# Kernel tuning notes

Hardware: AMD Instinct MI355X
Metric: run time of the kernel (lower is better)

The kernel has to match this reference:

```python
import jax, jax.numpy as jnp
import numpy as np

B, S, HID = 2, 2048, 1024
H, HKV, D = 16, 8, 128
G = H // HKV
EPS = 1e-6
ROPE_BASE = 1e6


def _rms_norm(x, w):
    # per-last-dim RMSNorm in fp32, matching QwenRMSNorm
    x32 = x.astype(jnp.float32)
    var = jnp.mean(x32 * x32, axis=-1, keepdims=True)
    return w * (x32 * jax.lax.rsqrt(var + EPS)).astype(x.dtype)


def _rotate_half(x):
    half = x.shape[-1] // 2
    return jnp.concatenate([-x[..., half:], x[..., :half]], axis=-1)


def setup_inputs() -> dict:
    key = jax.random.key(0)
    ks = jax.random.split(key, 6)
    return {
        "hidden_states": jax.random.normal(ks[0], (B, S, HID), dtype=jnp.float32),
        "position_ids": jnp.arange(S, dtype=jnp.int32),
        "Wq": jax.random.normal(ks[1], (HID, H * D), dtype=jnp.float32) * 0.02,
        "Wk": jax.random.normal(ks[2], (HID, HKV * D), dtype=jnp.float32) * 0.02,
        "Wv": jax.random.normal(ks[3], (HID, HKV * D), dtype=jnp.float32) * 0.02,
        "Wo": jax.random.normal(ks[4], (H * D, HID), dtype=jnp.float32) * 0.02,
        "q_norm_w": jnp.ones((D,), dtype=jnp.float32),
        "k_norm_w": jnp.ones((D,), dtype=jnp.float32),
    }


def reference(hidden_states, position_ids, Wq, Wk, Wv, Wo, q_norm_w, k_norm_w):
    b, s, _ = hidden_states.shape
    # projections
    q = (hidden_states @ Wq).reshape(b, s, H, D)
    k = (hidden_states @ Wk).reshape(b, s, HKV, D)
    v = (hidden_states @ Wv).reshape(b, s, HKV, D)
    # QK RMSNorm (per head_dim), then [B, heads, S, D]
    q = _rms_norm(q, q_norm_w).transpose(0, 2, 1, 3)
    k = _rms_norm(k, k_norm_w).transpose(0, 2, 1, 3)
    v = v.transpose(0, 2, 1, 3)
    # RoPE
    inv_freq = 1.0 / (ROPE_BASE ** (jnp.arange(0, D, 2, dtype=jnp.float32) / D))
    freqs = position_ids.astype(jnp.float32)[:, None] * inv_freq[None, :]  # [S, D/2]
    emb = jnp.concatenate([freqs, freqs], axis=-1)  # [S, D]
    cos = jnp.cos(emb)[None, None, :, :].astype(q.dtype)
    sin = jnp.sin(emb)[None, None, :, :].astype(q.dtype)
    q = q * cos + _rotate_half(q) * sin
    k = k * cos + _rotate_half(k) * sin
    # GQA attention without materializing repeated K/V:
    # q heads h = kh*G + g  <->  repeat_interleave(G, dim=1) of kv heads
    qg = q.reshape(b, HKV, G, s, D)
    scale = 1.0 / jnp.sqrt(jnp.asarray(D, dtype=q.dtype))
    scores = jnp.einsum('bhgqd,bhkd->bhgqk', qg, k) * scale  # [B,HKV,G,S,S]
    causal = jnp.tril(jnp.ones((s, s), dtype=bool))
    scores = jnp.where(causal[None, None, None, :, :], scores, jnp.finfo(scores.dtype).min)
    probs = jax.nn.softmax(scores, axis=-1)
    attn = jnp.einsum('bhgqk,bhkd->bhgqd', probs, v)  # [B,HKV,G,S,D]
    attn = attn.reshape(b, H, s, D).transpose(0, 2, 1, 3).reshape(b, s, H * D)
    out = attn @ Wo
    return out, k, v
```

## Files before the change

### kernel.cpp

```cpp
#include <hip/hip_runtime.h>

#define B_ 2
#define S_ 2048
#define HID_ 1024
#define H_ 16
#define HKV_ 8
#define D_ 128

typedef unsigned short u16;
typedef __attribute__((ext_vector_type(8))) short short8;
typedef __attribute__((ext_vector_type(4))) float f32x4;
typedef __attribute__((ext_vector_type(16))) float f32x16;
typedef __attribute__((ext_vector_type(2))) unsigned short u16x2;
typedef __attribute__((ext_vector_type(4))) unsigned short u16x4;
typedef const __attribute__((address_space(1))) void gvoid;
typedef __attribute__((address_space(3))) void svoid;

__device__ __forceinline__ u16 f2b(float f) {
  union { float f; unsigned u; } v; v.f = f;
  unsigned r = v.u + 0x7FFFu + ((v.u >> 16) & 1u);
  return (u16)(r >> 16);
}
__device__ __forceinline__ float b2f(u16 x) {
  union { unsigned u; float f; } v; v.u = ((unsigned)x) << 16; return v.f;
}

__device__ __forceinline__ float exp2_fast(float x) {
  float r; asm("v_exp_f32 %0, %1" : "=v"(r) : "v"(x)); return r;
}
__device__ __forceinline__ unsigned cvtpk_bf16(float lo, float hi) {
  unsigned r; asm("v_cvt_pk_bf16_f32 %0, %1, %2" : "=v"(r) : "v"(lo), "v"(hi)); return r;
}
__device__ __forceinline__ void vm_drain() {
  asm volatile("s_waitcnt vmcnt(0)" ::: "memory");
  __builtin_amdgcn_sched_barrier(0);
}

__global__ __launch_bounds__(256) void conv_bf16_kernel(const float* __restrict__ X,
                                                        u16* __restrict__ Y, int n4) {
  int i = blockIdx.x * 256 + threadIdx.x;
  if (i < n4) {
    const float4 v = ((const float4*)X)[i];
    u16x4 o = { f2b(v.x), f2b(v.y), f2b(v.z), f2b(v.w) };
    ((u16x4*)Y)[i] = o;
  }
}

template <bool PERM>
__global__ __launch_bounds__(256) void transpose_bf16_kernel(const float* __restrict__ W,
                                                             u16* __restrict__ Wt,
                                                             int K, int N) {
  __shared__ float t[32][33];
  const int nb = N >> 5;
  const int bx = blockIdx.x % nb;
  const int by = blockIdx.x / nb;
  const int tx = threadIdx.x & 31, ty = threadIdx.x >> 5;
#pragma unroll
  for (int i = 0; i < 32; i += 8)
    t[ty + i][tx] = W[(size_t)(by * 32 + ty + i) * N + bx * 32 + tx];
  __syncthreads();
#pragma unroll
  for (int i = 0; i < 32; i += 8) {
    int n = bx * 32 + ty + i;
    int nn;
    if (PERM) {
      int head = n >> 7, d = n & 127;
      int p = (d & 15) | (((d >> 6) & 1) << 4) | (((d >> 4) & 1) << 5) | (((d >> 5) & 1) << 6);
      nn = head * 128 + p;
    } else {
      nn = n;
    }
    Wt[(size_t)nn * K + by * 32 + tx] = f2b(t[tx][ty + i]);
  }
}

__global__ __launch_bounds__(256) void rope_table_kernel(const int* __restrict__ pid,
                                                         float* __restrict__ ct,
                                                         float* __restrict__ st) {
  int i = blockIdx.x * 256 + threadIdx.x;
  if (i >= 64 * S_) return;
  int f = i >> 11, s = i & 2047;
  double inv = exp2(-(double)f * (19.931568569324174 / 64.0));
  double ang = (double)pid[s] * inv;
  ct[i] = (float)cos(ang);
  st[i] = (float)sin(ang);
}

template <int M, int N, int K, int BM>
__global__ __launch_bounds__(256) void gemm_bt(const u16* __restrict__ A,
                                               const u16* __restrict__ Bt,
                                               float* __restrict__ C) {
  __shared__ u16 As[BM * 32];
  __shared__ u16 Bs[128 * 32];
  const int tid = threadIdx.x;
  const int w = tid >> 6;
  const int l = tid & 63;
  const int l15 = l & 15, lg = l >> 4;
  const int nbx = N / 128;
  const int bx = blockIdx.x % nbx, by = blockIdx.x / nbx;
  const int row0 = by * BM, col0 = bx * 128;
  const int wr = w >> 1, wc = w & 1;
  constexpr int MR = BM / 32;

  f32x4 acc[MR][4];
#pragma unroll
  for (int m = 0; m < MR; ++m)
#pragma unroll
    for (int n = 0; n < 4; ++n) acc[m][n] = (f32x4){0.f, 0.f, 0.f, 0.f};

  for (int k0 = 0; k0 < K; k0 += 32) {
    __syncthreads();
#pragma unroll
    for (int i = 0; i < BM / 64; ++i) {
      int c = i * 256 + tid;
      int r = c >> 2, cc = c & 3;
      const u16* sa = A + (size_t)(row0 + r) * K + k0 + cc * 8;
      __builtin_amdgcn_global_load_lds((gvoid*)sa, (svoid*)(As + (i * 256 + w * 64) * 8), 16, 0, 0);
    }
#pragma unroll
    for (int i = 0; i < 2; ++i) {
      int c = i * 256 + tid;
      int r = c >> 2, cc = c & 3;
      const u16* sb = Bt + (size_t)(col0 + r) * K + k0 + cc * 8;
      __builtin_amdgcn_global_load_lds((gvoid*)sb, (svoid*)(Bs + (i * 256 + w * 64) * 8), 16, 0, 0);
    }
    vm_drain();
    __syncthreads();
    short8 af[MR], bf[4];
#pragma unroll
    for (int m = 0; m < MR; ++m)
      af[m] = *(const short8*)(As + (wr * (BM / 2) + m * 16 + l15) * 32 + lg * 8);
#pragma unroll
    for (int n = 0; n < 4; ++n)
      bf[n] = *(const short8*)(Bs + (wc * 64 + n * 16 + l15) * 32 + lg * 8);
#pragma unroll
    for (int m = 0; m < MR; ++m)
#pragma unroll
      for (int n = 0; n < 4; ++n)
        acc[m][n] = __builtin_amdgcn_mfma_f32_16x16x32_bf16(af[m], bf[n], acc[m][n], 0, 0, 0);
  }
#pragma unroll
  for (int m = 0; m < MR; ++m)
#pragma unroll
    for (int n = 0; n < 4; ++n) {
      float* cp = C + (size_t)(row0 + wr * (BM / 2) + m * 16 + lg * 4) * N + col0 + wc * 64 + n * 16 + l15;
#pragma unroll
      for (int r = 0; r < 4; ++r) cp[(size_t)r * N] = acc[m][n][r];
    }
}

__global__ __launch_bounds__(256) void gemm_qkv_fused(const u16* __restrict__ A,
                                                      const u16* __restrict__ Bt,
                                                      const float* __restrict__ qnw,
                                                      const float* __restrict__ knw,
                                                      const float* __restrict__ ct_t,
                                                      const float* __restrict__ st_t,
                                                      u16* __restrict__ Qbb,
                                                      u16* __restrict__ Kbb,
                                                      float* __restrict__ kout,
                                                      float* __restrict__ vout,
                                                      u16* __restrict__ VTb) {
  constexpr int K = 1024;
  __shared__ u16 As[64 * 64];
  __shared__ u16 Bs[128 * 64];
  __shared__ float red[64][2];
  const int tid = threadIdx.x;
  const int w = tid >> 6;
  const int l = tid & 63;
  const int l15 = l & 15, lg = l >> 4;
  const int bx = blockIdx.x & 31, by = blockIdx.x >> 5;
  const int row0 = by * 64, col0 = bx * 128;
  const int wr = w >> 1, wc = w & 1;

  f32x4 acc[2][4];
#pragma unroll
  for (int m = 0; m < 2; ++m)
#pragma unroll
    for (int n = 0; n < 4; ++n) acc[m][n] = (f32x4){0.f, 0.f, 0.f, 0.f};

  for (int k0 = 0; k0 < K; k0 += 64) {
    __syncthreads();
#pragma unroll
    for (int i = 0; i < 2; ++i) {
      int c = i * 256 + tid;
      int r = c >> 3, cc = c & 7;
      int cs = cc ^ ((r ^ (r >> 3)) & 7);
      const u16* sa = A + (size_t)(row0 + r) * K + k0 + cs * 8;
      __builtin_amdgcn_global_load_lds((gvoid*)sa, (svoid*)(As + (i * 256 + w * 64) * 8), 16, 0, 0);
    }
#pragma unroll
    for (int i = 0; i < 4; ++i) {
      int c = i * 256 + tid;
      int r = c >> 3, cc = c & 7;
      int cs = cc ^ ((r ^ (r >> 3)) & 7);
      const u16* sb = Bt + (size_t)(col0 + r) * K + k0 + cs * 8;
      __builtin_amdgcn_global_load_lds((gvoid*)sb, (svoid*)(Bs + (i * 256 + w * 64) * 8), 16, 0, 0);
    }
    vm_drain();
    __syncthreads();
#pragma unroll
    for (int kk = 0; kk < 2; ++kk) {
      short8 af[2], bf[4];
#pragma unroll
      for (int m = 0; m < 2; ++m) {
        const int row = wr * 32 + m * 16 + l15;
        af[m] = *(const short8*)((const char*)As + row * 128 +
                                 (((kk * 4 + lg) ^ ((row ^ (row >> 3)) & 7)) << 4));
      }
#pragma unroll
      for (int n = 0; n < 4; ++n) {
        const int row = wc * 64 + n * 16 + l15;
        bf[n] = *(const short8*)((const char*)Bs + row * 128 +
                                 (((kk * 4 + lg) ^ ((row ^ (row >> 3)) & 7)) << 4));
      }
#pragma unroll
      for (int m = 0; m < 2; ++m)
#pragma unroll
        for (int n = 0; n < 4; ++n)
          acc[m][n] = __builtin_amdgcn_mfma_f32_16x16x32_bf16(af[m], bf[n], acc[m][n], 0, 0, 0);
    }
  }

  const int b_ = row0 >> 11;
  const int s0 = row0 & 2047;
  if (bx < 24) {
    float part[2][4];
#pragma unroll
    for (int m = 0; m < 2; ++m)
#pragma unroll
      for (int r = 0; r < 4; ++r) {
        float p = 0.f;
#pragma unroll
        for (int n = 0; n < 4; ++n) p += acc[m][n][r] * acc[m][n][r];
        part[m][r] = p;
      }
#pragma unroll
    for (int i = 1; i < 16; i <<= 1)
#pragma unroll
      for (int m = 0; m < 2; ++m)
#pragma unroll
        for (int r = 0; r < 4; ++r) part[m][r] += __shfl_xor(part[m][r], i, 64);
    if (l15 == 0) {
#pragma unroll
      for (int m = 0; m < 2; ++m)
#pragma unroll
        for (int r = 0; r < 4; ++r) red[wr * 32 + m * 16 + lg * 4 + r][wc] = part[m][r];
    }
    __syncthreads();

    const bool isQ = bx < 16;
    const int h = isQ ? bx : bx - 16;
    const float* nw = isQ ? qnw : knw;
    u16* outb = isQ ? Qbb : Kbb;
    const int NH = isQ ? 16 : 8;
#pragma unroll
    for (int np = 0; np < 2; ++np) {
      const int d_lo = l15 + 32 * wc + 16 * np;
      const float w_lo = nw[d_lo], w_hi = nw[d_lo + 64];
#pragma unroll
      for (int m = 0; m < 2; ++m) {
        const int sb = s0 + wr * 32 + m * 16 + lg * 4;
        const float4 cv = *(const float4*)(ct_t + d_lo * 2048 + sb);
        const float4 sv = *(const float4*)(st_t + d_lo * 2048 + sb);
#pragma unroll
        for (int r = 0; r < 4; ++r) {
          const int ro = wr * 32 + m * 16 + lg * 4 + r;
          const float tot = red[ro][0] + red[ro][1];
          const float rms = rsqrtf(tot * (1.0f / 128.0f) + 1e-6f);
          const float xl = acc[m][2 * np][r] * rms * w_lo;
          const float xh = acc[m][2 * np + 1][r] * rms * w_hi;
          const float cc = ((const float*)&cv)[r], ss = ((const float*)&sv)[r];
          const float ol = xl * cc - xh * ss;
          const float oh = xh * cc + xl * ss;
          const size_t base = ((size_t)(b_ * NH + h) * 2048 + sb + r) * 128;
          outb[base + d_lo] = f2b(ol);
          outb[base + d_lo + 64] = f2b(oh);
          if (!isQ) {
            kout[base + d_lo] = ol;
            kout[base + d_lo + 64] = oh;
          }
        }
      }
    }
  } else {
    const int h = bx - 24;
#pragma unroll
    for (int n = 0; n < 4; ++n) {
      const int d = wc * 64 + n * 16 + l15;
#pragma unroll
      for (int m = 0; m < 2; ++m) {
        const int sb = s0 + wr * 32 + m * 16 + lg * 4;
        u16x4 pk;
#pragma unroll
        for (int r = 0; r < 4; ++r) {
          const float x = acc[m][n][r];
          vout[((size_t)(b_ * 8 + h) * 2048 + sb + r) * 128 + d] = x;
          pk[r] = f2b(x);
        }
        *(u16x4*)(VTb + ((size_t)(b_ * 8 + h) * 128 + d) * 2048 + sb) = pk;
      }
    }
  }
}

__global__ __launch_bounds__(256, 2) void attn_kernel(const u16* __restrict__ Qb,
                                                      const u16* __restrict__ Kb,
                                                      const u16* __restrict__ VTb,
                                                      u16* __restrict__ Ab,
                                                      u16* __restrict__ Op,
                                                      float* __restrict__ Ml) {
  __shared__ u16 lds[2][16384];
  const int tid = threadIdx.x;
  const int w = tid >> 6, l = tid & 63;
  const int l31 = l & 31, hi = l >> 5;
  const int bid = blockIdx.x;
  const int half = bid & 1;
  const int pid = bid >> 1;
  const int b = pid >> 7;
  const int hh = (pid >> 3) & 15;
  const int p8 = pid & 7;
  const int hkv = hh >> 1;

  const u16* Kh = Kb + (size_t)(b * HKV_ + hkv) * S_ * 128;
  const u16* VTh = VTb + (size_t)(b * HKV_ + hkv) * 128 * S_;
  const float KSC = 0.12751740027f;
  int cur = 0;

  auto stage = [&](int kt, int buf) {
    const u16* Kp = Kh + (size_t)kt * 64 * 128;
    const u16* Vp = VTh + kt * 64;
    u16* Kd = &lds[buf][0];
    u16* Vd = &lds[buf][8192];
#pragma unroll
    for (int i = 0; i < 4; ++i) {
      int c = i * 256 + tid;
      int kr = c >> 4, kc = c & 15;
      int kcs = kc ^ ((kr ^ (kr >> 3)) & 15);
      __builtin_amdgcn_global_load_lds((gvoid*)(Kp + kr * 128 + kcs * 8),
                                       (svoid*)(Kd + (i * 256 + w * 64) * 8), 16, 0, 0);
      int vd = c >> 3, vc = c & 7;
      int vcs = vc ^ ((vd ^ (vd >> 3)) & 7);
      __builtin_amdgcn_global_load_lds((gvoid*)(Vp + (size_t)vd * S_ + vcs * 8),
                                       (svoid*)(Vd + (i * 256 + w * 64) * 8), 16, 0, 0);
    }
  };

  auto run_seg = [&](int pp, int kt0, int kt1, int mode) {
    const int q0 = pp * 128;
    const int ntp = 2 * (pp + 1);
    const int qrow = q0 + w * 32 + l31;

    short8 qf[8];
    {
      const u16* qp = Qb + ((size_t)(b * H_ + hh) * S_ + qrow) * 128 + hi * 8;
#pragma unroll
      for (int c = 0; c < 8; ++c) qf[c] = *(const short8*)(qp + c * 16);
    }

    float m_run = -1e30f, l_run = 0.f;
    f32x16 oacc[4];
#pragma unroll
    for (int n = 0; n < 4; ++n)
#pragma unroll
      for (int r = 0; r < 16; ++r) oacc[n][r] = 0.f;

    stage(kt0, cur);
    vm_drain();
    __syncthreads();
    for (int kt = kt0; kt < kt1; ++kt) {
      if (kt + 1 < kt1) stage(kt + 1, cur ^ 1);
      const u16* Kl = &lds[cur][0];
      const u16* Vl = &lds[cur][8192];
      const bool domask = (kt >= ntp - 2);

#pragma unroll
      for (int ts = 0; ts < 2; ++ts) {
        f32x16 stv;
#pragma unroll
        for (int r = 0; r < 16; ++r) stv[r] = 0.f;
        {
          const int row = ts * 32 + l31;
          const int rb = row * 256, sw = ((row ^ (row >> 3)) & 15) << 4;
          __builtin_amdgcn_s_setprio(1);
#pragma unroll
          for (int c = 0; c < 8; ++c) {
            short8 kf = *(const short8*)((const char*)Kl + rb + ((c * 32 + hi * 16) ^ sw));
            stv = __builtin_amdgcn_mfma_f32_32x32x16_bf16(kf, qf[c], stv, 0, 0, 0);
          }
          __builtin_amdgcn_s_setprio(0);
        }

        float pvv[16];
        float mx = -1e30f;
#pragma unroll
        for (int r = 0; r < 16; ++r) {
          float x = stv[r] * KSC;
          if (domask) {
            int kv = kt * 64 + ts * 32 + (r & 3) + 8 * (r >> 2) + 4 * hi;
            if (kv > qrow) x = -1e30f;
          }
          pvv[r] = x;
          mx = fmaxf(mx, x);
        }
        mx = fmaxf(mx, __shfl_xor(mx, 32, 64));

        if (__any(mx > m_run + 8.0f)) {
          float mnew = fmaxf(m_run, mx);
          float corr = exp2_fast(m_run - mnew);
          l_run *= corr;
          m_run = mnew;
#pragma unroll
          for (int r = 0; r < 16; ++r) {
            float cr = __shfl(corr, (r & 3) + 8 * (r >> 2) + 4 * hi, 64);
#pragma unroll
            for (int n = 0; n < 4; ++n) oacc[n][r] *= cr;
          }
        }

        float ls = 0.f;
#pragma unroll
        for (int r = 0; r < 16; ++r) {
          float p = exp2_fast(pvv[r] - m_run);
          pvv[r] = p;
          ls += p;
        }
        l_run += ls + __shfl_xor(ls, 32, 64);

        unsigned W[4][2], Wx[4][2];
#pragma unroll
        for (int g = 0; g < 4; ++g)
#pragma unroll
          for (int i = 0; i < 2; ++i) {
            W[g][i] = cvtpk_bf16(pvv[4 * g + 2 * i], pvv[4 * g + 2 * i + 1]);
            Wx[g][i] = __shfl_xor(W[g][i], 32, 64);
          }

        __builtin_amdgcn_s_setprio(1);
#pragma unroll
        for (int cc = 0; cc < 2; ++cc) {
          short8 paf;
          ((unsigned*)&paf)[0] = hi ? Wx[2 * cc + 1][0] : W[2 * cc][0];
          ((unsigned*)&paf)[1] = hi ? Wx[2 * cc + 1][1] : W[2 * cc][1];
          ((unsigned*)&paf)[2] = hi ? W[2 * cc + 1][0] : Wx[2 * cc][0];
          ((unsigned*)&paf)[3] = hi ? W[2 * cc + 1][1] : Wx[2 * cc][1];
          const int cp = ts * 2 + cc;
#pragma unroll
          for (int n = 0; n < 4; ++n) {
            const int d = n * 32 + l31;
            const int swv = ((d ^ (d >> 3)) & 7) << 4;
            short8 vf = *(const short8*)((const char*)Vl + d * 128 + ((cp * 32 + hi * 16) ^ swv));
            oacc[n] = __builtin_amdgcn_mfma_f32_32x32x16_bf16(paf, vf, oacc[n], 0, 0, 0);
          }
        }
        __builtin_amdgcn_s_setprio(0);
      }
      vm_drain();
      __syncthreads();
      cur ^= 1;
    }

    if (mode == 0) {
#pragma unroll
      for (int r = 0; r < 16; ++r) {
        const int ql = (r & 3) + 8 * (r >> 2) + 4 * hi;
        float lb = __shfl(l_run, ql, 64);
        float inv = 1.0f / lb;
        const int q = q0 + w * 32 + ql;
        u16* op = Ab + ((size_t)(b * S_) + q) * 2048 + hh * 128 + l31;
#pragma unroll
        for (int n = 0; n < 4; ++n) op[n * 32] = f2b(oacc[n][r] * inv);
      }
    } else {
      const int part = mode - 1;
      u16* ob = Op + ((size_t)(part * 256 + pid)) * 128 * 128;
#pragma unroll
      for (int r = 0; r < 16; ++r) {
        const int ql = (r & 3) + 8 * (r >> 2) + 4 * hi;
        const int qq = w * 32 + ql;
#pragma unroll
        for (int n = 0; n < 4; ++n) ob[qq * 128 + n * 32 + l31] = f2b(oacc[n][r]);
      }
      if (hi == 0) {
        float* mlb = Ml + ((size_t)(part * 256 + pid)) * 256;
        mlb[w * 32 + l31] = m_run;
        mlb[128 + w * 32 + l31] = l_run;
      }
    }
  };

  if (half == 0) {
    run_seg(p8, 0, 2 * p8 + 2, 0);
    run_seg(15 - p8, 0, 15 - 2 * p8, 1);
  } else {
    run_seg(15 - p8, 15 - 2 * p8, 32 - 2 * p8, 2);
  }
}

__global__ __launch_bounds__(256) void attn_combine_kernel(const u16* __restrict__ Op,
                                                           const float* __restrict__ Ml,
                                                           u16* __restrict__ Ab) {
  const int pid = blockIdx.x;
  const int b = pid >> 7, hh = (pid >> 3) & 15, p8 = pid & 7;
  const int pp = 15 - p8;
  const int q = threadIdx.x >> 1;
  const int d0 = (threadIdx.x & 1) * 64;
  const float* ml0 = Ml + (size_t)pid * 256;
  const float* ml1 = Ml + (size_t)(256 + pid) * 256;
  const float m0 = ml0[q], l0 = ml0[128 + q];
  const float m1 = ml1[q], l1 = ml1[128 + q];
  const float m = fmaxf(m0, m1);
  const float w0 = exp2_fast(m0 - m), w1 = exp2_fast(m1 - m);
  const float linv = 1.0f / (w0 * l0 + w1 * l1);
  const u16* o0 = Op + ((size_t)pid * 128 + q) * 128 + d0;
  const u16* o1 = Op + ((size_t)(256 + pid) * 128 + q) * 128 + d0;
  u16* ab = Ab + ((size_t)(b * S_) + pp * 128 + q) * 2048 + hh * 128 + d0;
#pragma unroll
  for (int c = 0; c < 8; ++c) {
    short8 a = *(const short8*)(o0 + c * 8);
    short8 bb = *(const short8*)(o1 + c * 8);
    short8 o;
#pragma unroll
    for (int j = 0; j < 8; ++j)
      o[j] = (short)f2b((w0 * b2f((u16)a[j]) + w1 * b2f((u16)bb[j])) * linv);
    *(short8*)(ab + c * 8) = o;
  }
}

extern "C" void kernel_launch(void* const* d_in, const int* in_sizes, int n_in,
                              void* d_out, int out_size, void* d_ws, size_t ws_size,
                              hipStream_t stream) {
  const float* hs  = (const float*)d_in[0];
  const int*   pid = (const int*)d_in[1];
  const float* Wq  = (const float*)d_in[2];
  const float* Wk  = (const float*)d_in[3];
  const float* Wv  = (const float*)d_in[4];
  const float* Wo  = (const float*)d_in[5];
  const float* qnw = (const float*)d_in[6];
  const float* knw = (const float*)d_in[7];

  float* out0 = (float*)d_out;
  float* kout = out0 + (size_t)B_ * HKV_ * S_ * D_;
  float* vout = kout + (size_t)B_ * HKV_ * S_ * D_;

  char* ws = (char*)d_ws;
  size_t off = 0;
  auto alloc = [&](size_t bytes) {
    void* p = ws + off;
    off += (bytes + 255) & ~(size_t)255;
    return p;
  };
  u16*   Xb    = (u16*)alloc((size_t)4096 * 1024 * 2);
  u16*   Wqkvt = (u16*)alloc((size_t)4096 * 1024 * 2);
  u16*   Wot   = (u16*)alloc((size_t)1024 * 2048 * 2);
  float* ct_t  = (float*)alloc((size_t)64 * 2048 * 4);
  float* st_t  = (float*)alloc((size_t)64 * 2048 * 4);
  u16*   Qbb   = (u16*)alloc((size_t)B_ * H_ * S_ * D_ * 2);
  u16*   Kbb   = (u16*)alloc((size_t)B_ * HKV_ * S_ * D_ * 2);
  u16*   VTb   = (u16*)alloc((size_t)B_ * HKV_ * D_ * S_ * 2);
  u16*   Ab    = (u16*)alloc((size_t)B_ * S_ * H_ * D_ * 2);
  u16*   Op    = (u16*)alloc((size_t)2 * 256 * 128 * 128 * 2);
  float* Ml    = (float*)alloc((size_t)2 * 256 * 256 * 4);

  conv_bf16_kernel<<<4096, 256, 0, stream>>>(hs, Xb, 4096 * 1024 / 4);
  transpose_bf16_kernel<true><<<(2048 / 32) * (1024 / 32), 256, 0, stream>>>(Wq, Wqkvt, 1024, 2048);
  transpose_bf16_kernel<true><<<(1024 / 32) * (1024 / 32), 256, 0, stream>>>(Wk, Wqkvt + (size_t)2048 * 1024, 1024, 1024);
  transpose_bf16_kernel<false><<<(1024 / 32) * (1024 / 32), 256, 0, stream>>>(Wv, Wqkvt + (size_t)3072 * 1024, 1024, 1024);
  transpose_bf16_kernel<false><<<(1024 / 32) * (2048 / 32), 256, 0, stream>>>(Wo, Wot, 2048, 1024);
  rope_table_kernel<<<512, 256, 0, stream>>>(pid, ct_t, st_t);

  gemm_qkv_fused<<<2048, 256, 0, stream>>>(Xb, Wqkvt, qnw, knw, ct_t, st_t,
                                           Qbb, Kbb, kout, vout, VTb);

  attn_kernel<<<512, 256, 0, stream>>>(Qbb, Kbb, VTb, Ab, Op, Ml);
  attn_combine_kernel<<<256, 256, 0, stream>>>(Op, Ml, Ab);

  gemm_bt<4096, 1024, 2048, 64><<<8 * 64, 256, 0, stream>>>(Ab, Wot, out0);
}
```

Measured before the change: 173.6 us.

## Double GEMM K-tile with XOR-swizzled LDS and split QK^T MFMA accumulators

The gemm_bt kernel now stages 64-wide K tiles instead of 32. This halves the number of barrier and drain iterations, and it stores the tiles with an XOR swizzle so the 16-byte fragment reads avoid LDS bank conflicts. In the attention kernel, the QK^T dot product is split across two independent MFMA accumulators that are summed afterwards, which breaks the serial dependency chain between back-to-back 32x32 MFMAs. The cost is doubled LDS use in the GEMM and extra accumulator registers plus adds in attention, which could reduce occupancy.

```diff
diff --git a/kernel.cpp b/kernel.cpp
--- a/kernel.cpp
+++ b/kernel.cpp
@@ -90,8 +90,8 @@
 __global__ __launch_bounds__(256) void gemm_bt(const u16* __restrict__ A,
                                                const u16* __restrict__ Bt,
                                                float* __restrict__ C) {
-  __shared__ u16 As[BM * 32];
-  __shared__ u16 Bs[128 * 32];
+  __shared__ u16 As[BM * 64];
+  __shared__ u16 Bs[128 * 64];
   const int tid = threadIdx.x;
   const int w = tid >> 6;
   const int l = tid & 63;
@@ -108,36 +108,47 @@
 #pragma unroll
     for (int n = 0; n < 4; ++n) acc[m][n] = (f32x4){0.f, 0.f, 0.f, 0.f};
 
-  for (int k0 = 0; k0 < K; k0 += 32) {
+  for (int k0 = 0; k0 < K; k0 += 64) {
     __syncthreads();
 #pragma unroll
-    for (int i = 0; i < BM / 64; ++i) {
+    for (int i = 0; i < BM / 32; ++i) {
       int c = i * 256 + tid;
-      int r = c >> 2, cc = c & 3;
-      const u16* sa = A + (size_t)(row0 + r) * K + k0 + cc * 8;
+      int r = c >> 3, cc = c & 7;
+      int cs = cc ^ ((r ^ (r >> 3)) & 7);
+      const u16* sa = A + (size_t)(row0 + r) * K + k0 + cs * 8;
       __builtin_amdgcn_global_load_lds((gvoid*)sa, (svoid*)(As + (i * 256 + w * 64) * 8), 16, 0, 0);
     }
 #pragma unroll
-    for (int i = 0; i < 2; ++i) {
+    for (int i = 0; i < 4; ++i) {
       int c = i * 256 + tid;
-      int r = c >> 2, cc = c & 3;
-      const u16* sb = Bt + (size_t)(col0 + r) * K + k0 + cc * 8;
+      int r = c >> 3, cc = c & 7;
+      int cs = cc ^ ((r ^ (r >> 3)) & 7);
+      const u16* sb = Bt + (size_t)(col0 + r) * K + k0 + cs * 8;
       __builtin_amdgcn_global_load_lds((gvoid*)sb, (svoid*)(Bs + (i * 256 + w * 64) * 8), 16, 0, 0);
     }
     vm_drain();
     __syncthreads();
-    short8 af[MR], bf[4];
-#pragma unroll
-    for (int m = 0; m < MR; ++m)
-      af[m] = *(const short8*)(As + (wr * (BM / 2) + m * 16 + l15) * 32 + lg * 8);
-#pragma unroll
-    for (int n = 0; n < 4; ++n)
-      bf[n] = *(const short8*)(Bs + (wc * 64 + n * 16 + l15) * 32 + lg * 8);
-#pragma unroll
-    for (int m = 0; m < MR; ++m)
-#pragma unroll
-      for (int n = 0; n < 4; ++n)
-        acc[m][n] = __builtin_amdgcn_mfma_f32_16x16x32_bf16(af[m], bf[n], acc[m][n], 0, 0, 0);
+#pragma unroll
+    for (int kk = 0; kk < 2; ++kk) {
+      short8 af[MR], bf[4];
+#pragma unroll
+      for (int m = 0; m < MR; ++m) {
+        const int row = wr * (BM / 2) + m * 16 + l15;
+        af[m] = *(const short8*)((const char*)As + row * 128 +
+                                 (((kk * 4 + lg) ^ ((row ^ (row >> 3)) & 7)) << 4));
+      }
+#pragma unroll
+      for (int n = 0; n < 4; ++n) {
+        const int row = wc * 64 + n * 16 + l15;
+        bf[n] = *(const short8*)((const char*)Bs + row * 128 +
+                                 (((kk * 4 + lg) ^ ((row ^ (row >> 3)) & 7)) << 4));
+      }
+#pragma unroll
+      for (int m = 0; m < MR; ++m)
+#pragma unroll
+        for (int n = 0; n < 4; ++n)
+          acc[m][n] = __builtin_amdgcn_mfma_f32_16x16x32_bf16(af[m], bf[n], acc[m][n], 0, 0, 0);
+    }
   }
 #pragma unroll
   for (int m = 0; m < MR; ++m)
@@ -375,9 +386,9 @@
 
 #pragma unroll
       for (int ts = 0; ts < 2; ++ts) {
-        f32x16 stv;
-#pragma unroll
-        for (int r = 0; r < 16; ++r) stv[r] = 0.f;
+        f32x16 stv0, stv1;
+#pragma unroll
+        for (int r = 0; r < 16; ++r) { stv0[r] = 0.f; stv1[r] = 0.f; }
         {
           const int row = ts * 32 + l31;
           const int rb = row * 256, sw = ((row ^ (row >> 3)) & 15) << 4;
@@ -385,7 +396,10 @@
 #pragma unroll
           for (int c = 0; c < 8; ++c) {
             short8 kf = *(const short8*)((const char*)Kl + rb + ((c * 32 + hi * 16) ^ sw));
-            stv = __builtin_amdgcn_mfma_f32_32x32x16_bf16(kf, qf[c], stv, 0, 0, 0);
+            if (c & 1)
+              stv1 = __builtin_amdgcn_mfma_f32_32x32x16_bf16(kf, qf[c], stv1, 0, 0, 0);
+            else
+              stv0 = __builtin_amdgcn_mfma_f32_32x32x16_bf16(kf, qf[c], stv0, 0, 0, 0);
           }
           __builtin_amdgcn_s_setprio(0);
         }
@@ -394,7 +408,7 @@
         float mx = -1e30f;
 #pragma unroll
         for (int r = 0; r < 16; ++r) {
-          float x = stv[r] * KSC;
+          float x = (stv0[r] + stv1[r]) * KSC;
           if (domask) {
             int kv = kt * 64 + ts * 32 + (r & 3) + 8 * (r >> 2) + 4 * hi;
             if (kv > qrow) x = -1e30f;
```

Measured after the change: 172.7 us. Within noise of the previous version (-0.5%).
